# Kernel optimization log

Measured on AMD Instinct MI355X. Metric: run time of the kernel, lower is better.

## Reference

```python
import jax, jax.numpy as jnp
import numpy as np

HIDDEN = 2048
N_HEADS = 16
N_KV_HEADS = 8
HEAD_DIM = 128
MROPE_SECTION = [8, 8, 24, 24]          # sums to HEAD_DIM // 2
ROPE_THETA = 10000.0
B, S, CTX = 4, 1024, 2048
# per-frequency section index (which of the 4 position streams drives each freq)
_SEC_IDX = np.repeat(np.arange(len(MROPE_SECTION)), MROPE_SECTION)  # (HEAD_DIM//2,)


def setup_inputs() -> dict:
    key = jax.random.key(0)
    ks = jax.random.split(key, 6)
    return {
        "hidden_states": jax.random.normal(ks[0], (B, S, HIDDEN), jnp.float32),
        "Wqkv": jax.random.normal(ks[1], (HIDDEN, (N_HEADS + 2 * N_KV_HEADS) * HEAD_DIM), jnp.float32) * 0.02,
        "Wo": jax.random.normal(ks[2], (N_HEADS * HEAD_DIM, HIDDEN), jnp.float32) * 0.02,
        "ctx_k": jax.random.normal(ks[3], (B, CTX, N_KV_HEADS, HEAD_DIM), jnp.float32),
        "ctx_v": jax.random.normal(ks[4], (B, CTX, N_KV_HEADS, HEAD_DIM), jnp.float32),
        "position_ids": jax.random.randint(ks[5], (len(MROPE_SECTION), S), 0, CTX + S, jnp.int32),
    }


def _mrope_cos_sin(position_ids):
    # position_ids: (n_sections, S) int -> cos/sin of shape (S, HEAD_DIM)
    half = HEAD_DIM // 2
    inv_freq = 1.0 / (ROPE_THETA ** (jnp.arange(0, half, dtype=jnp.float32) * 2.0 / HEAD_DIM))
    freqs = position_ids.astype(jnp.float32)[:, :, None] * inv_freq[None, None, :]  # (4, S, half)
    sec = jnp.asarray(_SEC_IDX)[None, None, :]                                       # (1, 1, half)
    f = jnp.take_along_axis(freqs, jnp.broadcast_to(sec, (1,) + freqs.shape[1:]), axis=0)[0]  # (S, half)
    emb = jnp.concatenate([f, f], axis=-1)  # (S, HEAD_DIM)
    return jnp.cos(emb), jnp.sin(emb)


def _rotate_half(x):
    h = x.shape[-1] // 2
    return jnp.concatenate([-x[..., h:], x[..., :h]], axis=-1)


def reference(hidden_states, Wqkv, Wo, ctx_k, ctx_v, position_ids):
    b, s, _ = hidden_states.shape
    q_size = N_HEADS * HEAD_DIM
    kv_size = N_KV_HEADS * HEAD_DIM
    qkv = hidden_states @ Wqkv  # (B, S, q+2kv)
    q = qkv[..., :q_size].reshape(b, s, N_HEADS, HEAD_DIM)
    k = qkv[..., q_size:q_size + kv_size].reshape(b, s, N_KV_HEADS, HEAD_DIM)
    v = qkv[..., q_size + kv_size:].reshape(b, s, N_KV_HEADS, HEAD_DIM)

    cos, sin = _mrope_cos_sin(position_ids)        # (S, D) each
    cos = cos[None, :, None, :]
    sin = sin[None, :, None, :]
    q = q * cos + _rotate_half(q) * sin
    k = k * cos + _rotate_half(k) * sin

    # KV-cache concat along sequence dim
    k = jnp.concatenate([ctx_k, k], axis=1)        # (B, CTX+S, KV, D)
    v = jnp.concatenate([ctx_v, v], axis=1)

    # GQA: expand kv heads to query heads
    rep = N_HEADS // N_KV_HEADS
    k = jnp.repeat(k, rep, axis=2)                 # (B, T, H, D)
    v = jnp.repeat(v, rep, axis=2)

    scale = HEAD_DIM ** -0.5
    scores = jnp.einsum("bqhd,bkhd->bhqk", q, k) * scale  # non-causal
    probs = jax.nn.softmax(scores, axis=-1)
    out = jnp.einsum("bhqk,bkhd->bqhd", probs, v)  # (B, S, H, D)
    out = out.reshape(b, s, N_HEADS * HEAD_DIM)
    return out @ Wo
```

## Files before the change

kernel.cpp:

```cpp
#include <hip/hip_runtime.h>
#include <hip/hip_bf16.h>
#include <stdint.h>

#define NH 16
#define NKV 8
#define HD 128
#define BB 4
#define SS 1024
#define CTXL 2048
#define LT 3072
#define HID 2048
#define QKVN 4096
#define MROWS 4096

typedef __hip_bfloat16 bf16;
using f32x4 = __attribute__((ext_vector_type(4))) float;
using s16x8 = __attribute__((ext_vector_type(8))) short;

#define MFMA(a, b, c) __builtin_amdgcn_mfma_f32_16x16x32_bf16((a), (b), (c), 0, 0, 0)

__device__ __forceinline__ void gload_lds16(const void* g, void* l) {
  __builtin_amdgcn_global_load_lds((const __attribute__((address_space(1))) void*)g,
                                   (__attribute__((address_space(3))) void*)l, 16, 0, 0);
}

__device__ __forceinline__ void store_bf8(bf16* dst, const float* f) {
  bf16 tmp[8];
#pragma unroll
  for (int j = 0; j < 8; ++j) tmp[j] = __float2bfloat16(f[j]);
  __builtin_memcpy((void*)dst, (const void*)tmp, 16);
}

__device__ __forceinline__ float bf2f(short x) {
  unsigned int u = ((unsigned int)(unsigned short)x) << 16;
  float f;
  __builtin_memcpy(&f, &u, 4);
  return f;
}

#define P1_CVT 4096
#define P1_WQ (P1_CVT + 8192)
#define P1_WO (P1_WQ + 4096)
#define P1_RT (P1_WO + 256)
#define P1_CK (P1_RT + 4096)
#define P1_CV (P1_CK + 8192)

__global__ void prep1(const float* __restrict__ hs, const float* __restrict__ Wqkv,
                      const float* __restrict__ Wo, const float* __restrict__ ck,
                      const float* __restrict__ cv, const int* __restrict__ pid,
                      bf16* __restrict__ Hb, bf16* __restrict__ WqT,
                      bf16* __restrict__ WoT, bf16* __restrict__ Kf,
                      bf16* __restrict__ Vt, float* __restrict__ cosT,
                      float* __restrict__ sinT) {
  __shared__ float tile[32][33];
  const int blk = blockIdx.x, thr = threadIdx.x;
  if (blk < P1_CVT) {
    size_t tid = (size_t)blk * 256 + thr;
    const float4* p = (const float4*)(hs + tid * 8);
    float4 a = p[0], b = p[1];
    float f[8] = {a.x, a.y, a.z, a.w, b.x, b.y, b.z, b.w};
    store_bf8(Hb + tid * 8, f);
  } else if (blk < P1_WQ) {
    int j = blk - P1_CVT;
    int c0 = (j & 127) * 32, r0 = (j >> 7) * 32;
    int tx = thr & 31, ty = thr >> 5;
#pragma unroll
    for (int i = 0; i < 32; i += 8)
      tile[ty + i][tx] = Wqkv[(size_t)(r0 + ty + i) * QKVN + c0 + tx];
    __syncthreads();
#pragma unroll
    for (int i = 0; i < 32; i += 8)
      WqT[(size_t)(c0 + ty + i) * HID + r0 + tx] = __float2bfloat16(tile[tx][ty + i]);
  } else if (blk < P1_WO) {
    int j = blk - P1_WQ;
    int c0 = (j & 63) * 32, r0 = (j >> 6) * 32;
    int tx = thr & 31, ty = thr >> 5;
#pragma unroll
    for (int i = 0; i < 32; i += 8)
      tile[ty + i][tx] = Wo[(size_t)(r0 + ty + i) * 2048 + c0 + tx];
    __syncthreads();
#pragma unroll
    for (int i = 0; i < 32; i += 8)
      WoT[(size_t)(c0 + ty + i) * 2048 + r0 + tx] = __float2bfloat16(tile[tx][ty + i]);
  } else if (blk < P1_RT) {
    int tid = (blk - P1_WO) * 256 + thr;
    int j = tid & 63, s = tid >> 6;
    int sec = (j < 8) ? 0 : (j < 16) ? 1 : (j < 40) ? 2 : 3;
    float pos = (float)pid[sec * SS + s];
    float inv = __expf(-(float)j * 0.14391156831212787f);
    float a = pos * inv;
    cosT[tid] = cosf(a);
    sinT[tid] = sinf(a);
  } else if (blk < P1_CK) {
    int tid = (blk - P1_RT) * 256 + thr;
    int d8 = tid & 15, l = (tid >> 4) & 2047, h = (tid >> 15) & 7, b = tid >> 18;
    const float* s = ck + (((size_t)b * CTXL + l) * NKV + h) * HD + d8 * 8;
    const float4* p = (const float4*)s;
    float4 a = p[0], bb = p[1];
    float f[8] = {a.x, a.y, a.z, a.w, bb.x, bb.y, bb.z, bb.w};
    store_bf8(Kf + (((size_t)(b * NKV + h)) * LT + l) * HD + d8 * 8, f);
  } else {
    int j = blk - P1_CK;
    int l0 = (j & 63) * 32, d0 = ((j >> 6) & 3) * 32;
    int bz = j >> 8, b = bz >> 3, h = bz & 7;
    int tx = thr & 31, ty = thr >> 5;
#pragma unroll
    for (int i = 0; i < 32; i += 8)
      tile[ty + i][tx] =
          cv[(((size_t)b * CTXL + l0 + ty + i) * NKV + h) * HD + d0 + tx];
    __syncthreads();
#pragma unroll
    for (int i = 0; i < 32; i += 8)
      Vt[(((size_t)(b * NKV + h)) * HD + d0 + ty + i) * LT + l0 + tx] =
          __float2bfloat16(tile[tx][ty + i]);
  }
}

__global__ void prep2(const bf16* __restrict__ qkv, const float* __restrict__ cosT,
                      const float* __restrict__ sinT, bf16* __restrict__ Kf,
                      bf16* __restrict__ Vt) {
  __shared__ float tile[32][33];
  const int blk = blockIdx.x, thr = threadIdx.x;
  if (blk < 8192) {
    int tid = blk * 256 + thr;
    int j = tid & 63, h = (tid >> 6) & 7, s = (tid >> 9) & 1023, b = tid >> 19;
    const bf16* src = qkv + ((size_t)b * SS + s) * QKVN + 2048 + h * HD;
    float x1 = __bfloat162float(src[j]), x2 = __bfloat162float(src[j + 64]);
    float c = cosT[s * 64 + j], sn = sinT[s * 64 + j];
    bf16* dst = Kf + (((size_t)(b * NKV + h)) * LT + CTXL + s) * HD;
    dst[j] = __float2bfloat16(x1 * c - x2 * sn);
    dst[j + 64] = __float2bfloat16(x2 * c + x1 * sn);
  } else {
    int j = blk - 8192;
    int s0 = (j & 31) * 32, d0 = ((j >> 5) & 3) * 32;
    int bz = j >> 7, b = bz >> 3, h = bz & 7;
    int tx = thr & 31, ty = thr >> 5;
#pragma unroll
    for (int i = 0; i < 32; i += 8)
      tile[ty + i][tx] = __bfloat162float(
          qkv[((size_t)b * SS + s0 + ty + i) * QKVN + 3072 + h * HD + d0 + tx]);
    __syncthreads();
#pragma unroll
    for (int i = 0; i < 32; i += 8)
      Vt[(((size_t)(b * NKV + h)) * HD + d0 + ty + i) * LT + CTXL + s0 + tx] =
          __float2bfloat16(tile[tx][ty + i]);
  }
}


template <typename OT>
__global__ __launch_bounds__(512, 1) void gemm_bt(const bf16* __restrict__ A,
                                                  const bf16* __restrict__ BT,
                                                  OT* __restrict__ C, int M, int N,
                                                  int K) {
  __shared__ __attribute__((aligned(16))) bf16 lA[3][256][64];
  __shared__ __attribute__((aligned(16))) bf16 lB[3][128][64];
  const int t = threadIdx.x;
  const int lane = t & 63, w = t >> 6;
  const int wr = w >> 1, wc = w & 1;
  const int lrow = lane & 15, kgrp = lane >> 4;
  const int rchk = lrow & 7;
  const int lin = blockIdx.y * gridDim.x + blockIdx.x;
  const int qq = (gridDim.x * gridDim.y) >> 3;
  const int swz = (lin & 7) * qq + (lin >> 3);
  const int bx = swz % gridDim.x, by = swz / gridDim.x;
  const int m0 = by * 256, n0 = bx * 128;
  const int srow = lane >> 3;
  const int schk = (lane & 7) ^ srow;
  const f32x4 fz = {0.f, 0.f, 0.f, 0.f};
  f32x4 acc[4][4];
#pragma unroll
  for (int i = 0; i < 4; ++i)
#pragma unroll
    for (int j = 0; j < 4; ++j) acc[i][j] = fz;
  const int NTK = K >> 6;

#define GSTAGE(ib, kt)                                                      \
  do {                                                                      \
    _Pragma("unroll") for (int c = 0; c < 4; ++c) {                         \
      int ra = c * 64 + w * 8 + srow;                                       \
      gload_lds16(A + (size_t)(m0 + ra) * K + (kt)*64 + schk * 8,           \
                  &lA[ib][c * 64 + w * 8][0]);                              \
    }                                                                       \
    _Pragma("unroll") for (int c = 0; c < 2; ++c) {                         \
      int rb = c * 64 + w * 8 + srow;                                       \
      gload_lds16(BT + (size_t)(n0 + rb) * K + (kt)*64 + schk * 8,          \
                  &lB[ib][c * 64 + w * 8][0]);                              \
    }                                                                       \
  } while (0)

  GSTAGE(0, 0);
  GSTAGE(1, 1);
  int ib = 0;
  for (int kt = 0; kt < NTK; ++kt) {
    if (kt + 1 < NTK)
      asm volatile("s_waitcnt vmcnt(6) lgkmcnt(0)" ::: "memory");
    else
      asm volatile("s_waitcnt vmcnt(0) lgkmcnt(0)" ::: "memory");
    __builtin_amdgcn_s_barrier();
    __builtin_amdgcn_sched_barrier(0);
    if (kt + 2 < NTK) {
      int ib2 = ib + 2;
      if (ib2 >= 3) ib2 -= 3;
      GSTAGE(ib2, kt + 2);
    }
#pragma unroll
    for (int kk = 0; kk < 2; ++kk) {
      s16x8 af[4], bf[4];
#pragma unroll
      for (int i = 0; i < 4; ++i)
        af[i] = *(const s16x8*)&lA[ib][wr * 64 + i * 16 + lrow]
                                     [(((kk << 2) + kgrp) ^ rchk) * 8];
#pragma unroll
      for (int j = 0; j < 4; ++j)
        bf[j] = *(const s16x8*)&lB[ib][wc * 64 + j * 16 + lrow]
                                     [(((kk << 2) + kgrp) ^ rchk) * 8];
      __builtin_amdgcn_s_setprio(1);
#pragma unroll
      for (int i = 0; i < 4; ++i)
#pragma unroll
        for (int j = 0; j < 4; ++j) acc[i][j] = MFMA(af[i], bf[j], acc[i][j]);
      __builtin_amdgcn_s_setprio(0);
    }
    ++ib;
    if (ib >= 3) ib = 0;
  }
#undef GSTAGE

#pragma unroll
  for (int i = 0; i < 4; ++i)
#pragma unroll
    for (int j = 0; j < 4; ++j)
#pragma unroll
      for (int r = 0; r < 4; ++r) {
        int row = m0 + wr * 64 + i * 16 + kgrp * 4 + r;
        int col = n0 + wc * 64 + j * 16 + lrow;
        float v = acc[i][j][r];
        if constexpr (sizeof(OT) == 2)
          C[(size_t)row * N + col] = __float2bfloat16(v);
        else
          C[(size_t)row * N + col] = v;
      }
}


#define PSTR 72
#define NT 48
#define SCALE2 0.1275174335919605f

__global__ __launch_bounds__(512, 2) void flash_attn(
    const bf16* __restrict__ qkv, const float* __restrict__ cosT,
    const float* __restrict__ sinT, const bf16* __restrict__ Kf,
    const bf16* __restrict__ Vt, bf16* __restrict__ O) {
  __shared__ __attribute__((aligned(16))) bf16 Kl[2][64][128];
  __shared__ __attribute__((aligned(16))) bf16 Vl[2][128][64];
  __shared__ __attribute__((aligned(16))) bf16 P_lds[8][32][PSTR];
  const int t = threadIdx.x, lane = t & 63, w = t >> 6;
  const int qb = blockIdx.x & 3, h = (blockIdx.x >> 2) & 15, b = blockIdx.x >> 6;
  const int hk = h >> 1;
  const int lrow = lane & 15, kgrp = lane >> 4;
  const bf16* Kp = Kf + (size_t)(b * NKV + hk) * LT * HD;
  const bf16* Vp = Vt + (size_t)(b * NKV + hk) * HD * LT;

  s16x8 qf[2][4];
#pragma unroll
  for (int f = 0; f < 2; ++f) {
    int srw_i = qb * 256 + w * 32 + f * 16 + lrow;
    const bf16* qrow = qkv + ((size_t)b * SS + srw_i) * QKVN + h * HD;
    s16x8 qr[4];
#pragma unroll
    for (int kd = 0; kd < 4; ++kd)
      qr[kd] = *(const s16x8*)&qrow[kd * 32 + kgrp * 8];
    const float* crow = cosT + srw_i * 64 + kgrp * 8;
    const float* srow = sinT + srw_i * 64 + kgrp * 8;
    float qv[4][8], cc[2][8], ssv[2][8];
#pragma unroll
    for (int kd = 0; kd < 4; ++kd)
#pragma unroll
      for (int j = 0; j < 8; ++j) qv[kd][j] = bf2f(qr[kd][j]);
#pragma unroll
    for (int g = 0; g < 2; ++g)
#pragma unroll
      for (int j = 0; j < 8; ++j) {
        cc[g][j] = crow[g * 32 + j];
        ssv[g][j] = srow[g * 32 + j];
      }
    bf16 o[4][8];
#pragma unroll
    for (int j = 0; j < 8; ++j) {
      o[0][j] = __float2bfloat16(qv[0][j] * cc[0][j] - qv[2][j] * ssv[0][j]);
      o[1][j] = __float2bfloat16(qv[1][j] * cc[1][j] - qv[3][j] * ssv[1][j]);
      o[2][j] = __float2bfloat16(qv[2][j] * cc[0][j] + qv[0][j] * ssv[0][j]);
      o[3][j] = __float2bfloat16(qv[3][j] * cc[1][j] + qv[1][j] * ssv[1][j]);
    }
#pragma unroll
    for (int kd = 0; kd < 4; ++kd) __builtin_memcpy(&qf[f][kd], o[kd], 16);
  }

  const f32x4 fz = {0.f, 0.f, 0.f, 0.f};
  f32x4 acc[2][8];
#pragma unroll
  for (int f = 0; f < 2; ++f)
#pragma unroll
    for (int i = 0; i < 8; ++i) acc[f][i] = fz;
  float m_[2] = {-1e30f, -1e30f}, l_[2] = {0.f, 0.f};

#define STAGE_K(buf, l0)                                                        \
  do {                                                                          \
    _Pragma("unroll") for (int c = 0; c < 2; ++c) {                             \
      int row = w * 8 + c * 4 + (lane >> 4);                                    \
      gload_lds16(Kp + (size_t)((l0) + row) * HD + ((lane & 15) ^ (row & 15)) * 8, \
                  &Kl[buf][w * 8 + c * 4][0]);                                  \
    }                                                                           \
  } while (0)
#define STAGE_V(buf, l0)                                                        \
  do {                                                                          \
    _Pragma("unroll") for (int c = 0; c < 2; ++c) {                             \
      int d = w * 16 + c * 8 + (lane >> 3);                                     \
      gload_lds16(Vp + (size_t)d * LT + (l0) + ((lane & 7) ^ (d & 7)) * 8,      \
                  &Vl[buf][w * 16 + c * 8][0]);                                 \
    }                                                                           \
  } while (0)

  STAGE_K(0, 0);
  STAGE_V(0, 0);
  __syncthreads();

  for (int tt = 0; tt < NT; ++tt) {
    const int cur = tt & 1;
    if (tt + 1 < NT) {
      STAGE_K(cur ^ 1, (tt + 1) * 64);
      STAGE_V(cur ^ 1, (tt + 1) * 64);
    }

    f32x4 sc[2][4];
#pragma unroll
    for (int f = 0; f < 2; ++f)
#pragma unroll
      for (int cf = 0; cf < 4; ++cf) sc[f][cf] = fz;
#pragma unroll
    for (int cf = 0; cf < 4; ++cf)
#pragma unroll
      for (int kd = 0; kd < 4; ++kd) {
        s16x8 kb =
            *(const s16x8*)&Kl[cur][cf * 16 + lrow][((kd * 4 + kgrp) ^ lrow) * 8];
#pragma unroll
        for (int f = 0; f < 2; ++f) sc[f][cf] = MFMA(kb, qf[f][kd], sc[f][cf]);
      }

    float mxv[2];
#pragma unroll
    for (int f = 0; f < 2; ++f) {
      float a0 = fmaxf(fmaxf(sc[f][0][0], sc[f][0][1]),
                       fmaxf(sc[f][0][2], sc[f][0][3]));
      float a1 = fmaxf(fmaxf(sc[f][1][0], sc[f][1][1]),
                       fmaxf(sc[f][1][2], sc[f][1][3]));
      float a2 = fmaxf(fmaxf(sc[f][2][0], sc[f][2][1]),
                       fmaxf(sc[f][2][2], sc[f][2][3]));
      float a3 = fmaxf(fmaxf(sc[f][3][0], sc[f][3][1]),
                       fmaxf(sc[f][3][2], sc[f][3][3]));
      float mx = fmaxf(fmaxf(a0, a1), fmaxf(a2, a3)) * SCALE2;
      mx = fmaxf(mx, __shfl_xor(mx, 16, 64));
      mx = fmaxf(mx, __shfl_xor(mx, 32, 64));
      mxv[f] = mx;
    }
    bool nb = (mxv[0] > m_[0] + 8.f) || (mxv[1] > m_[1] + 8.f);
    if (__any(nb)) {
#pragma unroll
      for (int f = 0; f < 2; ++f) {
        float mn = fmaxf(m_[f], mxv[f]);
        float so = exp2f(m_[f] - mn);
        m_[f] = mn;
        l_[f] *= so;
        float sob[4];
#pragma unroll
        for (int r = 0; r < 4; ++r) sob[r] = __shfl(so, kgrp * 4 + r, 16);
#pragma unroll
        for (int nd = 0; nd < 8; ++nd)
#pragma unroll
          for (int r = 0; r < 4; ++r) acc[f][nd][r] *= sob[r];
      }
    }
#pragma unroll
    for (int f = 0; f < 2; ++f) {
      float lp = 0.f;
#pragma unroll
      for (int cf = 0; cf < 4; ++cf) {
        bf16 pk[4];
#pragma unroll
        for (int r = 0; r < 4; ++r) {
          float p = exp2f(sc[f][cf][r] * SCALE2 - m_[f]);
          lp += p;
          pk[r] = __float2bfloat16(p);
        }
        __builtin_memcpy((void*)&P_lds[w][f * 16 + lrow][cf * 16 + kgrp * 4], pk, 8);
      }
      l_[f] += lp;
    }

    s16x8 pa[2][2];
#pragma unroll
    for (int f = 0; f < 2; ++f)
#pragma unroll
      for (int kc = 0; kc < 2; ++kc)
        pa[f][kc] = *(const s16x8*)&P_lds[w][f * 16 + lrow][kc * 32 + kgrp * 8];

#pragma unroll
    for (int nd = 0; nd < 8; ++nd)
#pragma unroll
      for (int kc = 0; kc < 2; ++kc) {
        s16x8 vb = *(const s16x8*)&Vl[cur][nd * 16 + lrow]
                                     [((kc * 4 + kgrp) ^ (lrow & 7)) * 8];
#pragma unroll
        for (int f = 0; f < 2; ++f) acc[f][nd] = MFMA(pa[f][kc], vb, acc[f][nd]);
      }
    __syncthreads();
  }
#undef STAGE_K
#undef STAGE_V

  float li[2][4];
#pragma unroll
  for (int f = 0; f < 2; ++f) {
    float lv = l_[f];
    lv += __shfl_xor(lv, 16, 64);
    lv += __shfl_xor(lv, 32, 64);
#pragma unroll
    for (int r = 0; r < 4; ++r) li[f][r] = 1.f / __shfl(lv, kgrp * 4 + r, 16);
  }
#pragma unroll
  for (int f = 0; f < 2; ++f)
#pragma unroll
    for (int nd = 0; nd < 8; ++nd)
#pragma unroll
      for (int r = 0; r < 4; ++r) {
        int row = qb * 256 + w * 32 + f * 16 + kgrp * 4 + r;
        O[((size_t)b * SS + row) * 2048 + h * HD + nd * 16 + lrow] =
            __float2bfloat16(acc[f][nd][r] * li[f][r]);
      }
}


extern "C" void kernel_launch(void* const* d_in, const int* in_sizes, int n_in,
                              void* d_out, int out_size, void* d_ws, size_t ws_size,
                              hipStream_t stream) {
  const float* hs = (const float*)d_in[0];
  const float* Wqkv = (const float*)d_in[1];
  const float* Wo = (const float*)d_in[2];
  const float* ctx_k = (const float*)d_in[3];
  const float* ctx_v = (const float*)d_in[4];
  const int* pid = (const int*)d_in[5];
  float* out = (float*)d_out;
  char* ws = (char*)d_ws;

  bf16* Hb = (bf16*)(ws);
  bf16* WqT = (bf16*)(ws + 16777216);
  bf16* WoT = (bf16*)(ws + 33554432);
  bf16* qkv = (bf16*)(ws + 41943040);
  bf16* Kfull = (bf16*)(ws + 92274688);
  bf16* Vt = (bf16*)(ws + 117440512);
  float* cosT = (float*)(ws + 142606336);
  float* sinT = (float*)(ws + 142606336 + 262144);
  bf16* attn = Hb;

  prep1<<<P1_CV, 256, 0, stream>>>(hs, Wqkv, Wo, ctx_k, ctx_v, pid, Hb, WqT, WoT,
                                   Kfull, Vt, cosT, sinT);
  gemm_bt<bf16><<<dim3(QKVN / 128, MROWS / 256), 512, 0, stream>>>(
      Hb, WqT, qkv, MROWS, QKVN, HID);
  prep2<<<12288, 256, 0, stream>>>(qkv, cosT, sinT, Kfull, Vt);
  flash_attn<<<256, 512, 0, stream>>>(qkv, cosT, sinT, Kfull, Vt, attn);
  gemm_bt<float><<<dim3(2048 / 128, MROWS / 256), 512, 0, stream>>>(
      attn, WoT, out, MROWS, 2048, HID);
}
```

Before: 340.0 us.

## Use 128-wide KV tiles with split V staging and head-paired block order

The flash attention loop now processes 128 keys per iteration instead of 64, which halves the number of iterations and barriers. K stays double-buffered, while V uses a single 128x128 buffer that is loaded at the start of each iteration and consumed after a mid-loop barrier. The PV product is split into two 64-key halves so that P can reuse the existing LDS scratch. Block IDs are remapped so the two query heads sharing a KV head sit next to each other, which should improve L2 reuse of K and V. The costs are higher register pressure from 16 score accumulators and V load latency that is no longer prefetched a full iteration ahead.

```diff
diff --git a/kernel.cpp b/kernel.cpp
--- a/kernel.cpp
+++ b/kernel.cpp
@@ -147,7 +147,6 @@
   }
 }
 
-
 template <typename OT>
 __global__ __launch_bounds__(512, 1) void gemm_bt(const bf16* __restrict__ A,
                                                   const bf16* __restrict__ BT,
@@ -245,19 +244,22 @@
 
 
 #define PSTR 72
-#define NT 48
+#define KVB 128
+#define NTT 24
 #define SCALE2 0.1275174335919605f
 
 __global__ __launch_bounds__(512, 2) void flash_attn(
     const bf16* __restrict__ qkv, const float* __restrict__ cosT,
     const float* __restrict__ sinT, const bf16* __restrict__ Kf,
     const bf16* __restrict__ Vt, bf16* __restrict__ O) {
-  __shared__ __attribute__((aligned(16))) bf16 Kl[2][64][128];
-  __shared__ __attribute__((aligned(16))) bf16 Vl[2][128][64];
+  __shared__ __attribute__((aligned(16))) bf16 Kl[2][128][128];
+  __shared__ __attribute__((aligned(16))) bf16 Vl[128][128];
   __shared__ __attribute__((aligned(16))) bf16 P_lds[8][32][PSTR];
   const int t = threadIdx.x, lane = t & 63, w = t >> 6;
-  const int qb = blockIdx.x & 3, h = (blockIdx.x >> 2) & 15, b = blockIdx.x >> 6;
-  const int hk = h >> 1;
+  const int id = blockIdx.x;
+  const int b = id >> 6, hk = id & 7;
+  const int h = (hk << 1) | ((id >> 5) & 1);
+  const int qb = (id >> 3) & 3;
   const int lrow = lane & 15, kgrp = lane >> 4;
   const bf16* Kp = Kf + (size_t)(b * NKV + hk) * LT * HD;
   const bf16* Vp = Vt + (size_t)(b * NKV + hk) * HD * LT;
@@ -307,39 +309,36 @@
 
 #define STAGE_K(buf, l0)                                                        \
   do {                                                                          \
-    _Pragma("unroll") for (int c = 0; c < 2; ++c) {                             \
-      int row = w * 8 + c * 4 + (lane >> 4);                                    \
+    _Pragma("unroll") for (int c = 0; c < 4; ++c) {                             \
+      int row = w * 16 + c * 4 + (lane >> 4);                                   \
       gload_lds16(Kp + (size_t)((l0) + row) * HD + ((lane & 15) ^ (row & 15)) * 8, \
-                  &Kl[buf][w * 8 + c * 4][0]);                                  \
+                  &Kl[buf][w * 16 + c * 4][0]);                                 \
     }                                                                           \
   } while (0)
-#define STAGE_V(buf, l0)                                                        \
+#define STAGE_V(l0)                                                             \
   do {                                                                          \
-    _Pragma("unroll") for (int c = 0; c < 2; ++c) {                             \
-      int d = w * 16 + c * 8 + (lane >> 3);                                     \
-      gload_lds16(Vp + (size_t)d * LT + (l0) + ((lane & 7) ^ (d & 7)) * 8,      \
-                  &Vl[buf][w * 16 + c * 8][0]);                                 \
+    _Pragma("unroll") for (int c = 0; c < 4; ++c) {                             \
+      int d = w * 16 + c * 4 + (lane >> 4);                                     \
+      gload_lds16(Vp + (size_t)d * LT + (l0) + ((lane & 15) ^ (d & 15)) * 8,    \
+                  &Vl[w * 16 + c * 4][0]);                                      \
     }                                                                           \
   } while (0)
 
   STAGE_K(0, 0);
-  STAGE_V(0, 0);
   __syncthreads();
 
-  for (int tt = 0; tt < NT; ++tt) {
+  for (int tt = 0; tt < NTT; ++tt) {
     const int cur = tt & 1;
-    if (tt + 1 < NT) {
-      STAGE_K(cur ^ 1, (tt + 1) * 64);
-      STAGE_V(cur ^ 1, (tt + 1) * 64);
-    }
-
-    f32x4 sc[2][4];
+    STAGE_V(tt * KVB);
+    if (tt + 1 < NTT) STAGE_K(cur ^ 1, (tt + 1) * KVB);
+
+    f32x4 sc[2][8];
 #pragma unroll
     for (int f = 0; f < 2; ++f)
 #pragma unroll
-      for (int cf = 0; cf < 4; ++cf) sc[f][cf] = fz;
-#pragma unroll
-    for (int cf = 0; cf < 4; ++cf)
+      for (int cf = 0; cf < 8; ++cf) sc[f][cf] = fz;
+#pragma unroll
+    for (int cf = 0; cf < 8; ++cf)
 #pragma unroll
       for (int kd = 0; kd < 4; ++kd) {
         s16x8 kb =
@@ -351,15 +350,12 @@
     float mxv[2];
 #pragma unroll
     for (int f = 0; f < 2; ++f) {
-      float a0 = fmaxf(fmaxf(sc[f][0][0], sc[f][0][1]),
-                       fmaxf(sc[f][0][2], sc[f][0][3]));
-      float a1 = fmaxf(fmaxf(sc[f][1][0], sc[f][1][1]),
-                       fmaxf(sc[f][1][2], sc[f][1][3]));
-      float a2 = fmaxf(fmaxf(sc[f][2][0], sc[f][2][1]),
-                       fmaxf(sc[f][2][2], sc[f][2][3]));
-      float a3 = fmaxf(fmaxf(sc[f][3][0], sc[f][3][1]),
-                       fmaxf(sc[f][3][2], sc[f][3][3]));
-      float mx = fmaxf(fmaxf(a0, a1), fmaxf(a2, a3)) * SCALE2;
+      float mx = sc[f][0][0];
+#pragma unroll
+      for (int cf = 0; cf < 8; ++cf)
+#pragma unroll
+        for (int r = 0; r < 4; ++r) mx = fmaxf(mx, sc[f][cf][r]);
+      mx *= SCALE2;
       mx = fmaxf(mx, __shfl_xor(mx, 16, 64));
       mx = fmaxf(mx, __shfl_xor(mx, 32, 64));
       mxv[f] = mx;
@@ -381,23 +377,21 @@
           for (int r = 0; r < 4; ++r) acc[f][nd][r] *= sob[r];
       }
     }
-#pragma unroll
-    for (int f = 0; f < 2; ++f) {
-      float lp = 0.f;
+
+    float lp[2] = {0.f, 0.f};
+#pragma unroll
+    for (int f = 0; f < 2; ++f)
 #pragma unroll
       for (int cf = 0; cf < 4; ++cf) {
         bf16 pk[4];
 #pragma unroll
         for (int r = 0; r < 4; ++r) {
           float p = exp2f(sc[f][cf][r] * SCALE2 - m_[f]);
-          lp += p;
+          lp[f] += p;
           pk[r] = __float2bfloat16(p);
         }
         __builtin_memcpy((void*)&P_lds[w][f * 16 + lrow][cf * 16 + kgrp * 4], pk, 8);
       }
-      l_[f] += lp;
-    }
-
     s16x8 pa[2][2];
 #pragma unroll
     for (int f = 0; f < 2; ++f)
@@ -405,12 +399,45 @@
       for (int kc = 0; kc < 2; ++kc)
         pa[f][kc] = *(const s16x8*)&P_lds[w][f * 16 + lrow][kc * 32 + kgrp * 8];
 
+    __syncthreads();
+
 #pragma unroll
     for (int nd = 0; nd < 8; ++nd)
 #pragma unroll
       for (int kc = 0; kc < 2; ++kc) {
-        s16x8 vb = *(const s16x8*)&Vl[cur][nd * 16 + lrow]
-                                     [((kc * 4 + kgrp) ^ (lrow & 7)) * 8];
+        s16x8 vb = *(const s16x8*)&Vl[nd * 16 + lrow]
+                                     [((kc * 4 + kgrp) ^ lrow) * 8];
+#pragma unroll
+        for (int f = 0; f < 2; ++f) acc[f][nd] = MFMA(pa[f][kc], vb, acc[f][nd]);
+      }
+
+#pragma unroll
+    for (int f = 0; f < 2; ++f)
+#pragma unroll
+      for (int cf = 4; cf < 8; ++cf) {
+        bf16 pk[4];
+#pragma unroll
+        for (int r = 0; r < 4; ++r) {
+          float p = exp2f(sc[f][cf][r] * SCALE2 - m_[f]);
+          lp[f] += p;
+          pk[r] = __float2bfloat16(p);
+        }
+        __builtin_memcpy(
+            (void*)&P_lds[w][f * 16 + lrow][(cf - 4) * 16 + kgrp * 4], pk, 8);
+      }
+#pragma unroll
+    for (int f = 0; f < 2; ++f) {
+      l_[f] += lp[f];
+#pragma unroll
+      for (int kc = 0; kc < 2; ++kc)
+        pa[f][kc] = *(const s16x8*)&P_lds[w][f * 16 + lrow][kc * 32 + kgrp * 8];
+    }
+#pragma unroll
+    for (int nd = 0; nd < 8; ++nd)
+#pragma unroll
+      for (int kc = 0; kc < 2; ++kc) {
+        s16x8 vb = *(const s16x8*)&Vl[nd * 16 + lrow]
+                                     [((8 + kc * 4 + kgrp) ^ lrow) * 8];
 #pragma unroll
         for (int f = 0; f < 2; ++f) acc[f][nd] = MFMA(pa[f][kc], vb, acc[f][nd]);
       }
```

New measurement: 325.8 us. 1.04x faster.
